# Performance work log

Measured on AMD Instinct MI355X. Metric: run time of the kernel, lower is better.

## Reference

```python
import jax, jax.numpy as jnp
import numpy as np

EMBED = 1024
HEADS = 16
HEAD_DIM = EMBED // HEADS
FFN_DIM = 4096
SEQ = 2048
BATCH = 2
EPS = 1e-5


def setup_inputs() -> dict:
    key = jax.random.key(0)
    ks = jax.random.split(key, 13)
    s = lambda n: 1.0 / np.sqrt(n)
    return {
        "x": jax.random.normal(ks[0], (BATCH, SEQ, EMBED), jnp.float32),
        # qkv projection (stored as [in, out])
        "w_qkv": jax.random.normal(ks[1], (EMBED, 3 * EMBED), jnp.float32) * s(EMBED),
        "b_qkv": jax.random.normal(ks[2], (3 * EMBED,), jnp.float32) * 0.02,
        "w_out": jax.random.normal(ks[3], (EMBED, EMBED), jnp.float32) * s(EMBED),
        "b_out": jax.random.normal(ks[4], (EMBED,), jnp.float32) * 0.02,
        # FFN
        "w_up": jax.random.normal(ks[5], (EMBED, FFN_DIM), jnp.float32) * s(EMBED),
        "b_up": jax.random.normal(ks[6], (FFN_DIM,), jnp.float32) * 0.02,
        "w_down": jax.random.normal(ks[7], (FFN_DIM, EMBED), jnp.float32) * s(FFN_DIM),
        "b_down": jax.random.normal(ks[8], (EMBED,), jnp.float32) * 0.02,
        # LayerNorms
        "g1": jnp.ones((EMBED,), jnp.float32),
        "be1": jnp.zeros((EMBED,), jnp.float32),
        "g2": jnp.ones((EMBED,), jnp.float32),
        "be2": jnp.zeros((EMBED,), jnp.float32),
    }


def _layernorm(x, g, b):
    mu = jnp.mean(x, axis=-1, keepdims=True)
    var = jnp.mean(jnp.square(x - mu), axis=-1, keepdims=True)
    return (x - mu) * jax.lax.rsqrt(var + EPS) * g + b


def reference(x, w_qkv, b_qkv, w_out, b_out, w_up, b_up, w_down, b_down, g1, be1, g2, be2):
    B, S, E = x.shape
    qkv = (x @ w_qkv + b_qkv).reshape(B, S, 3, HEADS, HEAD_DIM)
    qkv = jnp.transpose(qkv, (2, 0, 3, 1, 4))
    q, k, v = qkv[0], qkv[1], qkv[2]
    scale = 1.0 / jnp.sqrt(jnp.float32(HEAD_DIM))
    attn = jnp.einsum("bhqd,bhkd->bhqk", q, k) * scale  # [B,H,S,S]
    causal = jnp.tril(jnp.ones((S, S), bool))
    attn = jnp.where(causal, attn, -jnp.inf)
    attn = jax.nn.softmax(attn, axis=-1)
    out = jnp.einsum("bhqk,bhkd->bhqd", attn, v)  # [B,H,S,D]
    out = jnp.transpose(out, (0, 2, 1, 3)).reshape(B, S, E)
    attn_out = out @ w_out + b_out
    x = _layernorm(x + attn_out, g1, be1)
    ffn_out = jax.nn.relu(x @ w_up + b_up) @ w_down + b_down
    return _layernorm(x + ffn_out, g2, be2)
```

## Files before the change

kernel.cpp:

```cpp
#include <hip/hip_runtime.h>
#include <hip/hip_bf16.h>

#define EMBED 1024
#define HEADS 16
#define HDIM 64
#define FFN 4096
#define SEQ 2048
#define BATCH 2
#define MTOT (BATCH*SEQ)
#define QSCALE 0.1803368801111137f

typedef __attribute__((ext_vector_type(8))) short bf16x8;
typedef __attribute__((ext_vector_type(4))) float f32x4;
typedef __attribute__((ext_vector_type(16))) float f32x16;
typedef unsigned short u16;
typedef unsigned int u32;

__device__ __forceinline__ u16 f2bf(float f) {
  union { float f; unsigned u; } v; v.f = f;
  unsigned r = v.u + 0x7FFFu + ((v.u >> 16) & 1u);
  return (u16)(r >> 16);
}

__device__ __forceinline__ void async_ld16(const void* g, void* l) {
  __builtin_amdgcn_global_load_lds((const __attribute__((address_space(1))) void*)g,
                                   (__attribute__((address_space(3))) void*)l,
                                   16, 0, 0);
}

__device__ __forceinline__ void qkv_scatter(u16* qp, u16* kp, u16* vp,
                                            int row, int col, float v) {
  const int which = col >> 10, hh = (col >> 6) & 15, d = col & 63;
  const int bb = row >> 11, ss = row & 2047;
  const int bh = bb * 16 + hh;
  if (which == 0) {
    v *= QSCALE;
    size_t idx = ((((size_t)bh * 64 + (ss >> 5)) * 4 + (d >> 4)) << 9)
               + (((ss & 31) + 32 * ((d >> 3) & 1)) << 3) + (d & 7);
    qp[idx] = f2bf(v);
  } else if (which == 1) {
    size_t idx = ((((size_t)bh * 32 + (ss >> 6)) * 8 + (d >> 4) * 2 + ((ss >> 5) & 1)) << 9)
               + (((ss & 31) + 32 * ((d >> 3) & 1)) << 3) + (d & 7);
    kp[idx] = f2bf(v);
  } else {
    size_t idx = ((((size_t)bh * 32 + (ss >> 6)) * 8 + ((ss & 63) >> 4) * 2 + (d >> 5)) << 9)
               + (((d & 31) + 32 * ((ss >> 3) & 1)) << 3) + (ss & 7);
    vp[idx] = f2bf(v);
  }
}

__global__ __launch_bounds__(256) void k_cvt(const float* __restrict__ in,
                                             u16* __restrict__ out, int n4) {
  int i = blockIdx.x * 256 + threadIdx.x;
  int st = gridDim.x * 256;
  for (; i < n4; i += st) {
    float4 v = ((const float4*)in)[i];
    ushort4 o;
    o.x = f2bf(v.x); o.y = f2bf(v.y); o.z = f2bf(v.z); o.w = f2bf(v.w);
    ((ushort4*)out)[i] = o;
  }
}

__global__ __launch_bounds__(256) void k_tr(const float* __restrict__ w,
                                            u16* __restrict__ wT, int K, int N) {
  __shared__ u16 tile[32][33];
  int n0 = blockIdx.x * 32, k0 = blockIdx.y * 32;
  int tx = threadIdx.x, ty = threadIdx.y;
  #pragma unroll
  for (int i = 0; i < 4; ++i) {
    int k = k0 + ty + i * 8;
    tile[ty + i * 8][tx] = f2bf(w[(size_t)k * N + n0 + tx]);
  }
  __syncthreads();
  #pragma unroll
  for (int i = 0; i < 4; ++i) {
    int n = n0 + ty + i * 8;
    wT[(size_t)n * K + k0 + tx] = tile[tx][ty + i * 8];
  }
}

template <int OMODE, bool RELU>
__global__ __launch_bounds__(512) void k_gemm8(
    const u16* __restrict__ A, const u16* __restrict__ BT,
    const float* __restrict__ bias,
    void* __restrict__ out0, void* __restrict__ out1, void* __restrict__ out2,
    int M, int N, int K, int ldk) {
  __shared__ __align__(16) u16 As[2][2][128 * 64];
  __shared__ __align__(16) u16 Bs[2][2][128 * 64];
  const int tid = threadIdx.x;
  const int lane = tid & 63, g = lane >> 4, li = lane & 15;
  const int wid = tid >> 6, wm = wid >> 2, wn = wid & 3;

  const int gx = gridDim.x;
  const int nwg = gx * gridDim.y;
  const int flat = blockIdx.y * gx + blockIdx.x;
  const int cpx = nwg >> 3;
  const int swz = (flat & 7) * cpx + (flat >> 3);
  const int m0 = (swz / gx) * 256, n0 = (swz % gx) * 256;
  const int kchunk = blockIdx.z * K;

  f32x4 acc[8][4] = {};

  const u16* Ablk = A + (size_t)m0 * ldk + kchunk;
  const u16* Bblk = BT + (size_t)n0 * ldk + kchunk;
  const int trow = tid >> 3;
  const int sc = (tid & 7) ^ (trow & 7);

  auto stageA = [&](int buf, int h, int kt) {
    #pragma unroll
    for (int r = 0; r < 2; ++r)
      async_ld16(Ablk + (size_t)(h * 64 + r * 128 + trow) * ldk + kt + sc * 8,
                 &As[buf][h][0] + r * 4096 + tid * 8);
  };
  auto stageB = [&](int buf, int h, int kt) {
    #pragma unroll
    for (int r = 0; r < 2; ++r) {
      const int p = trow + r * 64;
      async_ld16(Bblk + (size_t)(((p >> 5) << 6) + h * 32 + (p & 31)) * ldk + kt + sc * 8,
                 &Bs[buf][h][0] + r * 4096 + tid * 8);
    }
  };

#define VM4_ asm volatile("s_waitcnt vmcnt(4)" ::: "memory")
#define VM2_ asm volatile("s_waitcnt vmcnt(2)" ::: "memory")
#define VM0_ asm volatile("s_waitcnt vmcnt(0)" ::: "memory")
#define VMN_
#define GP8(IH, JH, VMSTMT, STAGE_STMT) do {                                   \
    bf16x8 a_[4][2], b_[2][2];                                                 \
    _Pragma("unroll")                                                          \
    for (int i2 = 0; i2 < 4; ++i2) {                                           \
      const int pa = wm * 64 + i2 * 16 + li;                                   \
      _Pragma("unroll")                                                        \
      for (int ks = 0; ks < 2; ++ks)                                           \
        a_[i2][ks] = *(const bf16x8*)(&As[cur][IH][0] + pa * 64 +              \
                                      (((ks * 4 + g) ^ (li & 7)) * 8));        \
    }                                                                          \
    _Pragma("unroll")                                                          \
    for (int j2 = 0; j2 < 2; ++j2) {                                           \
      const int pb = wn * 32 + j2 * 16 + li;                                   \
      _Pragma("unroll")                                                        \
      for (int ks = 0; ks < 2; ++ks)                                           \
        b_[j2][ks] = *(const bf16x8*)(&Bs[cur][JH][0] + pb * 64 +              \
                                      (((ks * 4 + g) ^ (li & 7)) * 8));        \
    }                                                                          \
    STAGE_STMT;                                                                \
    VMSTMT;                                                                    \
    __builtin_amdgcn_s_barrier();                                              \
    asm volatile("s_waitcnt lgkmcnt(0)" ::: "memory");                         \
    __builtin_amdgcn_sched_barrier(0);                                         \
    __builtin_amdgcn_s_setprio(1);                                             \
    _Pragma("unroll")                                                          \
    for (int ks = 0; ks < 2; ++ks)                                             \
      _Pragma("unroll")                                                        \
      for (int i2 = 0; i2 < 4; ++i2)                                           \
        _Pragma("unroll")                                                      \
        for (int j2 = 0; j2 < 2; ++j2)                                         \
          acc[IH * 4 + i2][JH * 2 + j2] = __builtin_amdgcn_mfma_f32_16x16x32_bf16( \
              a_[i2][ks], b_[j2][ks], acc[IH * 4 + i2][JH * 2 + j2], 0, 0, 0); \
    __builtin_amdgcn_s_setprio(0);                                             \
    asm volatile("" ::: "memory");                                             \
  } while (0)

  stageA(0, 0, 0); stageB(0, 0, 0); stageA(0, 1, 0); stageB(0, 1, 0);
  VM4_;
  __builtin_amdgcn_s_barrier();
  asm volatile("" ::: "memory");

  int cur = 0;
  const int nkt = K >> 6;
  for (int t = 0; t < nkt - 1; ++t) {
    const int kn = (t + 1) * 64;
    GP8(0, 0, VM4_, stageA(cur ^ 1, 0, kn));
    GP8(1, 0, VM4_, stageB(cur ^ 1, 0, kn));
    GP8(0, 1, VMN_, stageA(cur ^ 1, 1, kn));
    GP8(1, 1, VM4_, stageB(cur ^ 1, 1, kn));
    cur ^= 1;
  }
  GP8(0, 0, VM2_, );
  GP8(1, 0, VM0_, );
  GP8(0, 1, VMN_, );
  GP8(1, 1, VMN_, );
#undef GP8
#undef VM4_
#undef VM2_
#undef VM0_
#undef VMN_

  float bcol[4];
  #pragma unroll
  for (int j = 0; j < 4; ++j)
    bcol[j] = (OMODE == 3) ? 0.f : bias[n0 + wn * 64 + j * 16 + li];

  #pragma unroll
  for (int i = 0; i < 8; ++i) {
    #pragma unroll
    for (int j = 0; j < 4; ++j) {
      #pragma unroll
      for (int r = 0; r < 4; ++r) {
        int row = m0 + wm * 128 + i * 16 + g * 4 + r;
        int col = n0 + wn * 64 + j * 16 + li;
        float v = acc[i][j][r] + bcol[j];
        if (RELU) v = fmaxf(v, 0.f);
        if (OMODE == 0) {
          ((u16*)out0)[(size_t)row * N + col] = f2bf(v);
        } else if (OMODE == 3) {
          ((float*)out0)[(size_t)blockIdx.z * M * N + (size_t)row * N + col] = v;
        } else {
          qkv_scatter((u16*)out0, (u16*)out1, (u16*)out2, row, col, v);
        }
      }
    }
  }
}

template <bool RELU>
__global__ __launch_bounds__(512) void k_gemmD(
    const u16* __restrict__ A, const u16* __restrict__ BT,
    const float* __restrict__ bias, float* __restrict__ out,
    int M, int N, int K) {
  __shared__ __align__(16) u16 As[4][2][64 * 64];
  __shared__ __align__(16) u16 Bs[4][2][64 * 64];
  const int tid = threadIdx.x;
  const int lane = tid & 63, g = lane >> 4, li = lane & 15;
  const int wid = tid >> 6, wm = wid >> 2, wn = wid & 3;

  const int gx = gridDim.x;
  const int nwg = gx * gridDim.y;
  const int flat = blockIdx.y * gx + blockIdx.x;
  const int cpx = nwg >> 3;
  const int swz = (flat & 7) * cpx + (flat >> 3);
  const int m0 = (swz / gx) * 128, n0 = (swz % gx) * 128;

  f32x4 acc[4][2] = {};

  const u16* Ablk = A + (size_t)m0 * K;
  const u16* Bblk = BT + (size_t)n0 * K;
  const int p = tid >> 3;
  const int c = (tid & 7) ^ (p & 7);

  auto stageAll = [&](int buf, int kt) {
    {
      const int grow = (p >> 5) * 64 + 0 * 32 + (p & 31);
      async_ld16(Ablk + (size_t)grow * K + kt + c * 8, &As[buf][0][0] + tid * 8);
    }
    {
      const int grow = (p >> 4) * 32 + 0 * 16 + (p & 15);
      async_ld16(Bblk + (size_t)grow * K + kt + c * 8, &Bs[buf][0][0] + tid * 8);
    }
    {
      const int grow = (p >> 4) * 32 + 1 * 16 + (p & 15);
      async_ld16(Bblk + (size_t)grow * K + kt + c * 8, &Bs[buf][1][0] + tid * 8);
    }
    {
      const int grow = (p >> 5) * 64 + 1 * 32 + (p & 31);
      async_ld16(Ablk + (size_t)grow * K + kt + c * 8, &As[buf][1][0] + tid * 8);
    }
  };

#define GATE(n) asm volatile("s_waitcnt vmcnt(" #n ")" ::: "memory")
  stageAll(0, 0);
  stageAll(1, 64);
  GATE(5);
  __builtin_amdgcn_s_barrier();
  asm volatile("" ::: "memory");

  const int nkt = K >> 6;
  const int pa0 = wm * 32 + li, pa1 = wm * 32 + 16 + li;
  const int pb = wn * 16 + li;
  for (int t = 0; t < nkt; ++t) {
    const int buf = t & 3;
    bf16x8 a_[2][2], b_[2][2];
    #pragma unroll
    for (int ks = 0; ks < 2; ++ks) {
      a_[0][ks] = *(const bf16x8*)(&As[buf][0][0] + pa0 * 64 + (((ks * 4 + g) ^ (pa0 & 7)) * 8));
      a_[1][ks] = *(const bf16x8*)(&As[buf][0][0] + pa1 * 64 + (((ks * 4 + g) ^ (pa1 & 7)) * 8));
      b_[0][ks] = *(const bf16x8*)(&Bs[buf][0][0] + pb * 64 + (((ks * 4 + g) ^ (pb & 7)) * 8));
      b_[1][ks] = *(const bf16x8*)(&Bs[buf][1][0] + pb * 64 + (((ks * 4 + g) ^ (pb & 7)) * 8));
    }
    if (t + 2 < nkt) {
      stageAll((t + 2) & 3, (t + 2) * 64);
      GATE(8);
    } else if (t + 1 < nkt) {
      GATE(4);
    } else {
      GATE(0);
    }
    __builtin_amdgcn_s_barrier();
    asm volatile("s_waitcnt lgkmcnt(0)" ::: "memory");
    __builtin_amdgcn_sched_barrier(0);
    __builtin_amdgcn_s_setprio(1);
    #pragma unroll
    for (int ks = 0; ks < 2; ++ks)
      #pragma unroll
      for (int i2l = 0; i2l < 2; ++i2l)
        #pragma unroll
        for (int j2 = 0; j2 < 2; ++j2)
          acc[i2l][j2] = __builtin_amdgcn_mfma_f32_16x16x32_bf16(
              a_[i2l][ks], b_[j2][ks], acc[i2l][j2], 0, 0, 0);
    __builtin_amdgcn_s_setprio(0);
    asm volatile("" ::: "memory");
    #pragma unroll
    for (int ks = 0; ks < 2; ++ks) {
      a_[0][ks] = *(const bf16x8*)(&As[buf][1][0] + pa0 * 64 + (((ks * 4 + g) ^ (pa0 & 7)) * 8));
      a_[1][ks] = *(const bf16x8*)(&As[buf][1][0] + pa1 * 64 + (((ks * 4 + g) ^ (pa1 & 7)) * 8));
    }
    if (t + 2 < nkt)      GATE(5);
    else if (t + 1 < nkt) GATE(1);
    __builtin_amdgcn_s_barrier();
    asm volatile("s_waitcnt lgkmcnt(0)" ::: "memory");
    __builtin_amdgcn_sched_barrier(0);
    __builtin_amdgcn_s_setprio(1);
    #pragma unroll
    for (int ks = 0; ks < 2; ++ks)
      #pragma unroll
      for (int i2l = 0; i2l < 2; ++i2l)
        #pragma unroll
        for (int j2 = 0; j2 < 2; ++j2)
          acc[2 + i2l][j2] = __builtin_amdgcn_mfma_f32_16x16x32_bf16(
              a_[i2l][ks], b_[j2][ks], acc[2 + i2l][j2], 0, 0, 0);
    __builtin_amdgcn_s_setprio(0);
    asm volatile("" ::: "memory");
  }
#undef GATE

  float bcol[2];
  #pragma unroll
  for (int j = 0; j < 2; ++j) bcol[j] = bias[n0 + wn * 32 + j * 16 + li];

  #pragma unroll
  for (int i = 0; i < 4; ++i) {
    #pragma unroll
    for (int j = 0; j < 2; ++j) {
      #pragma unroll
      for (int r = 0; r < 4; ++r) {
        int row = m0 + wm * 64 + i * 16 + g * 4 + r;
        int col = n0 + wn * 32 + j * 16 + li;
        float v = acc[i][j][r] + bcol[j];
        if (RELU) v = fmaxf(v, 0.f);
        out[(size_t)row * N + col] = v;
      }
    }
  }
}

__global__ __launch_bounds__(256, 3) void k_attn7(
    const u16* __restrict__ Qp, const u16* __restrict__ Kp,
    const u16* __restrict__ Vp, u16* __restrict__ ctx) {
  const int bh = blockIdx.x;
  const int t32 = 63 - (int)blockIdx.y;
  const int b = bh >> 4, h = bh & 15;
  const int tid = threadIdx.x;
  const int wid = tid >> 6, lane = tid & 63;
  const int ql = lane & 31, hl = lane >> 5;

  __shared__ __align__(16) float mrg[3][64][34];

  const int wq0 = t32 * 32;
  const int qg = wq0 + ql;
  const int nt = ((wq0 + 31) >> 6) + 1;

  bf16x8 qf[4];
  {
    const u16* qpb = Qp + ((((size_t)bh * 64 + t32) * 4) << 9) + lane * 8;
    #pragma unroll
    for (int d4 = 0; d4 < 4; ++d4)
      qf[d4] = *(const bf16x8*)(qpb + (d4 << 9));
  }

  const u16* kbase = Kp + (((size_t)bh * 32) << 12) + lane * 8;
  const u16* vbase = Vp + (((size_t)bh * 32) << 12) + lane * 8;

  f32x16 o0 = {}, o1 = {};
  float m_run = -1e30f, l_run = 0.f;

  for (int kt = wid; kt < nt; kt += 4) {
    const bool kh1 = (kt * 64 + 32 <= wq0 + 31);
    const bool domask = (kt * 64 + (kh1 ? 63 : 31) > wq0);
    const u16* kb_ = kbase + ((size_t)kt << 12);
    const u16* vb_ = vbase + ((size_t)kt << 12);

    bf16x8 kf0[4], kf1[4];
    #pragma unroll
    for (int d4 = 0; d4 < 4; ++d4) {
      kf0[d4] = *(const bf16x8*)(kb_ + ((d4 * 2 + 0) << 9));
      if (kh1) kf1[d4] = *(const bf16x8*)(kb_ + ((d4 * 2 + 1) << 9));
    }
    bf16x8 vf0[4], vf1[4];
    #pragma unroll
    for (int t = 0; t < 4; ++t)
      if (t < 2 || kh1) {
        vf0[t] = *(const bf16x8*)(vb_ + ((t * 2 + 0) << 9));
        vf1[t] = *(const bf16x8*)(vb_ + ((t * 2 + 1) << 9));
      }

    f32x16 S0 = {}, S1 = {};
    #pragma unroll
    for (int d4 = 0; d4 < 4; ++d4)
      S0 = __builtin_amdgcn_mfma_f32_32x32x16_bf16(kf0[d4], qf[d4], S0, 0, 0, 0);
    if (kh1) {
      #pragma unroll
      for (int d4 = 0; d4 < 4; ++d4)
        S1 = __builtin_amdgcn_mfma_f32_32x32x16_bf16(kf1[d4], qf[d4], S1, 0, 0, 0);
    }

    if (domask) {
      const int qrel = qg - kt * 64 - 4 * hl;
      #pragma unroll
      for (int r = 0; r < 16; ++r) {
        const int kc = (r & 3) + 8 * (r >> 2);
        S0[r] = (kc <= qrel) ? S0[r] : -3.0e38f;
      }
      if (kh1) {
        #pragma unroll
        for (int r = 0; r < 16; ++r) {
          const int kc = 32 + (r & 3) + 8 * (r >> 2);
          S1[r] = (kc <= qrel) ? S1[r] : -3.0e38f;
        }
      }
    }

    float mt = -3.0e38f;
    #pragma unroll
    for (int r = 0; r < 16; ++r) mt = fmaxf(mt, S0[r]);
    if (kh1) {
      #pragma unroll
      for (int r = 0; r < 16; ++r) mt = fmaxf(mt, S1[r]);
    }
    mt = fmaxf(mt, __shfl_xor(mt, 32, 64));

    if (!__all(mt <= m_run + 8.0f)) {
      const float mn = fmaxf(m_run, mt);
      const float alpha = exp2f(m_run - mn);
      l_run *= alpha;
      o0 *= alpha;
      o1 *= alpha;
      m_run = mn;
    }
    float sum = 0.f;
    #pragma unroll
    for (int r = 0; r < 16; ++r) { S0[r] = exp2f(S0[r] - m_run); sum += S0[r]; }
    if (kh1) {
      #pragma unroll
      for (int r = 0; r < 16; ++r) { S1[r] = exp2f(S1[r] - m_run); sum += S1[r]; }
    }
    sum += __shfl_xor(sum, 32, 64);
    l_run += sum;

    u32 pk[2][8], sw[2][8];
    #pragma unroll
    for (int m = 0; m < 4; ++m) {
      asm("v_cvt_pk_bf16_f32 %0, %1, %2" : "=v"(pk[0][2*m])   : "v"(S0[4*m+0]), "v"(S0[4*m+1]));
      asm("v_cvt_pk_bf16_f32 %0, %1, %2" : "=v"(pk[0][2*m+1]) : "v"(S0[4*m+2]), "v"(S0[4*m+3]));
    }
    #pragma unroll
    for (int i = 0; i < 8; ++i) sw[0][i] = __shfl_xor(pk[0][i], 32, 64);
    if (kh1) {
      #pragma unroll
      for (int m = 0; m < 4; ++m) {
        asm("v_cvt_pk_bf16_f32 %0, %1, %2" : "=v"(pk[1][2*m])   : "v"(S1[4*m+0]), "v"(S1[4*m+1]));
        asm("v_cvt_pk_bf16_f32 %0, %1, %2" : "=v"(pk[1][2*m+1]) : "v"(S1[4*m+2]), "v"(S1[4*m+3]));
      }
      #pragma unroll
      for (int i = 0; i < 8; ++i) sw[1][i] = __shfl_xor(pk[1][i], 32, 64);
    }

    #pragma unroll
    for (int t = 0; t < 4; ++t) {
      if (t < 2 || kh1) {
        const int c = t >> 1, m0 = 2 * (t & 1), m1 = m0 + 1;
        union { u32 u[4]; bf16x8 v; } pf;
        pf.u[0] = hl ? sw[c][2*m1]   : pk[c][2*m0];
        pf.u[1] = hl ? sw[c][2*m1+1] : pk[c][2*m0+1];
        pf.u[2] = hl ? pk[c][2*m1]   : sw[c][2*m0];
        pf.u[3] = hl ? pk[c][2*m1+1] : sw[c][2*m0+1];
        o0 = __builtin_amdgcn_mfma_f32_32x32x16_bf16(vf0[t], pf.v, o0, 0, 0, 0);
        o1 = __builtin_amdgcn_mfma_f32_32x32x16_bf16(vf1[t], pf.v, o1, 0, 0, 0);
      }
    }
  }

  if (wid > 0) {
    float* pq = &mrg[wid - 1][lane][0];
    *(f32x16*)(pq) = o0;
    *(f32x16*)(pq + 16) = o1;
    pq[32] = m_run;
    pq[33] = l_run;
  }
  __syncthreads();
  if (wid > 0) return;

  float M = m_run;
  #pragma unroll
  for (int w = 0; w < 3; ++w) M = fmaxf(M, mrg[w][lane][32]);
  const float fa = exp2f(m_run - M);
  f32x16 acc0 = o0 * fa, acc1 = o1 * fa;
  float L = l_run * fa;
  #pragma unroll
  for (int w = 0; w < 3; ++w) {
    const float* pq = &mrg[w][lane][0];
    const float fw = exp2f(pq[32] - M);
    L += pq[33] * fw;
    f32x16 t0 = *(const f32x16*)(pq);
    f32x16 t1 = *(const f32x16*)(pq + 16);
    acc0 += t0 * fw;
    acc1 += t1 * fw;
  }
  const float inv = 1.f / L;

  u16* outp = ctx + (size_t)(b * SEQ + qg) * EMBED + h * HDIM + 4 * hl;
  #pragma unroll
  for (int m = 0; m < 4; ++m) {
    ushort4 s0v, s1v;
    s0v.x = f2bf(acc0[4*m+0] * inv); s0v.y = f2bf(acc0[4*m+1] * inv);
    s0v.z = f2bf(acc0[4*m+2] * inv); s0v.w = f2bf(acc0[4*m+3] * inv);
    *(ushort4*)(outp + 8 * m) = s0v;
    s1v.x = f2bf(acc1[4*m+0] * inv); s1v.y = f2bf(acc1[4*m+1] * inv);
    s1v.z = f2bf(acc1[4*m+2] * inv); s1v.w = f2bf(acc1[4*m+3] * inv);
    *(ushort4*)(outp + 32 + 8 * m) = s1v;
  }
}

__global__ __launch_bounds__(256) void k_add_ln(
    const float* __restrict__ a, const float* __restrict__ bmat,
    const float* __restrict__ gam, const float* __restrict__ bet,
    float* __restrict__ outf, u16* __restrict__ outb) {
  const int row = blockIdx.x;
  const int t = threadIdx.x;
  __shared__ float red[8];
  float4 va = ((const float4*)(a + (size_t)row * EMBED))[t];
  float4 vb = ((const float4*)(bmat + (size_t)row * EMBED))[t];
  float s0 = va.x + vb.x, s1 = va.y + vb.y, s2 = va.z + vb.z, s3 = va.w + vb.w;
  float sum = s0 + s1 + s2 + s3;
  float sq = s0 * s0 + s1 * s1 + s2 * s2 + s3 * s3;
  #pragma unroll
  for (int m = 1; m < 64; m <<= 1) {
    sum += __shfl_xor(sum, m, 64);
    sq += __shfl_xor(sq, m, 64);
  }
  int wid = t >> 6;
  if ((t & 63) == 0) { red[wid] = sum; red[4 + wid] = sq; }
  __syncthreads();
  sum = red[0] + red[1] + red[2] + red[3];
  sq = red[4] + red[5] + red[6] + red[7];
  float mean = sum * (1.f / EMBED);
  float var = sq * (1.f / EMBED) - mean * mean;
  float rstd = rsqrtf(var + 1e-5f);
  float4 gv = ((const float4*)gam)[t], bev = ((const float4*)bet)[t];
  float y0 = (s0 - mean) * rstd * gv.x + bev.x;
  float y1 = (s1 - mean) * rstd * gv.y + bev.y;
  float y2 = (s2 - mean) * rstd * gv.z + bev.z;
  float y3 = (s3 - mean) * rstd * gv.w + bev.w;
  if (outf) {
    float4 o; o.x = y0; o.y = y1; o.z = y2; o.w = y3;
    ((float4*)(outf + (size_t)row * EMBED))[t] = o;
  }
  if (outb) {
    ushort4 ob; ob.x = f2bf(y0); ob.y = f2bf(y1); ob.z = f2bf(y2); ob.w = f2bf(y3);
    ((ushort4*)(outb + (size_t)row * EMBED))[t] = ob;
  }
}

__global__ __launch_bounds__(256) void k_add_ln4(
    const float* __restrict__ a, const float* __restrict__ parts,
    const float* __restrict__ bias,
    const float* __restrict__ gam, const float* __restrict__ bet,
    float* __restrict__ outf) {
  const int row = blockIdx.x;
  const int t = threadIdx.x;
  __shared__ float red[8];
  float4 va = ((const float4*)(a + (size_t)row * EMBED))[t];
  float4 bv = ((const float4*)bias)[t];
  float s0 = va.x + bv.x, s1 = va.y + bv.y, s2 = va.z + bv.z, s3 = va.w + bv.w;
  #pragma unroll
  for (int c = 0; c < 4; ++c) {
    float4 pv = ((const float4*)(parts + (size_t)c * MTOT * EMBED + (size_t)row * EMBED))[t];
    s0 += pv.x; s1 += pv.y; s2 += pv.z; s3 += pv.w;
  }
  float sum = s0 + s1 + s2 + s3;
  float sq = s0 * s0 + s1 * s1 + s2 * s2 + s3 * s3;
  #pragma unroll
  for (int m = 1; m < 64; m <<= 1) {
    sum += __shfl_xor(sum, m, 64);
    sq += __shfl_xor(sq, m, 64);
  }
  int wid = t >> 6;
  if ((t & 63) == 0) { red[wid] = sum; red[4 + wid] = sq; }
  __syncthreads();
  sum = red[0] + red[1] + red[2] + red[3];
  sq = red[4] + red[5] + red[6] + red[7];
  float mean = sum * (1.f / EMBED);
  float var = sq * (1.f / EMBED) - mean * mean;
  float rstd = rsqrtf(var + 1e-5f);
  float4 gv = ((const float4*)gam)[t], bev = ((const float4*)bet)[t];
  float4 o;
  o.x = (s0 - mean) * rstd * gv.x + bev.x;
  o.y = (s1 - mean) * rstd * gv.y + bev.y;
  o.z = (s2 - mean) * rstd * gv.z + bev.z;
  o.w = (s3 - mean) * rstd * gv.w + bev.w;
  ((float4*)(outf + (size_t)row * EMBED))[t] = o;
}

extern "C" void kernel_launch(void* const* d_in, const int* in_sizes, int n_in,
                              void* d_out, int out_size, void* d_ws, size_t ws_size,
                              hipStream_t stream) {
  const float* x      = (const float*)d_in[0];
  const float* w_qkv  = (const float*)d_in[1];
  const float* b_qkv  = (const float*)d_in[2];
  const float* w_out  = (const float*)d_in[3];
  const float* b_out  = (const float*)d_in[4];
  const float* w_up   = (const float*)d_in[5];
  const float* b_up   = (const float*)d_in[6];
  const float* w_down = (const float*)d_in[7];
  const float* b_down = (const float*)d_in[8];
  const float* g1  = (const float*)d_in[9];
  const float* be1 = (const float*)d_in[10];
  const float* g2  = (const float*)d_in[11];
  const float* be2 = (const float*)d_in[12];

  char* ws = (char*)d_ws;
  size_t off = 0;
  auto alloc = [&](size_t bytes) { void* p = ws + off; off += (bytes + 255) & ~(size_t)255; return p; };

  u16* xb     = (u16*)alloc((size_t)MTOT * EMBED * 2);
  u16* wqkvT  = (u16*)alloc((size_t)3 * EMBED * EMBED * 2);
  u16* woutT  = (u16*)alloc((size_t)EMBED * EMBED * 2);
  u16* wupT   = (u16*)alloc((size_t)FFN * EMBED * 2);
  u16* wdownT = (u16*)alloc((size_t)EMBED * FFN * 2);
  u16* qp     = (u16*)alloc((size_t)MTOT * EMBED * 2);
  u16* kp     = (u16*)alloc((size_t)MTOT * EMBED * 2);
  u16* vp     = (u16*)alloc((size_t)MTOT * EMBED * 2);
  u16* ctx    = (u16*)alloc((size_t)MTOT * EMBED * 2);
  float* attn_proj = (float*)alloc((size_t)MTOT * EMBED * 4);
  float* y_f32     = (float*)alloc((size_t)MTOT * EMBED * 4);
  u16* y_bf16      = (u16*)alloc((size_t)MTOT * EMBED * 2);
  u16* hmid        = (u16*)alloc((size_t)MTOT * FFN * 2);
  float* fparts    = (float*)alloc((size_t)4 * MTOT * EMBED * 4);

  dim3 trb(32, 8);
  k_cvt<<<2048, 256, 0, stream>>>(x, xb, MTOT * EMBED / 4);
  k_tr<<<dim3(3 * EMBED / 32, EMBED / 32), trb, 0, stream>>>(w_qkv, wqkvT, EMBED, 3 * EMBED);
  k_tr<<<dim3(EMBED / 32, EMBED / 32), trb, 0, stream>>>(w_out, woutT, EMBED, EMBED);
  k_tr<<<dim3(FFN / 32, EMBED / 32), trb, 0, stream>>>(w_up, wupT, EMBED, FFN);
  k_tr<<<dim3(EMBED / 32, FFN / 32), trb, 0, stream>>>(w_down, wdownT, FFN, EMBED);

  k_gemm8<2, false><<<dim3(3 * EMBED / 256, MTOT / 256), 512, 0, stream>>>(
      xb, wqkvT, b_qkv, qp, kp, vp, MTOT, 3 * EMBED, EMBED, EMBED);

  k_attn7<<<dim3(BATCH * HEADS, 64), 256, 0, stream>>>(qp, kp, vp, ctx);

  k_gemmD<false><<<dim3(EMBED / 128, MTOT / 128), 512, 0, stream>>>(
      ctx, woutT, b_out, attn_proj, MTOT, EMBED, EMBED);

  k_add_ln<<<MTOT, 256, 0, stream>>>(x, attn_proj, g1, be1, y_f32, y_bf16);

  k_gemm8<0, true><<<dim3(FFN / 256, MTOT / 256), 512, 0, stream>>>(
      y_bf16, wupT, b_up, hmid, nullptr, nullptr, MTOT, FFN, EMBED, EMBED);

  k_gemm8<3, false><<<dim3(EMBED / 256, MTOT / 256, 4), 512, 0, stream>>>(
      hmid, wdownT, nullptr, fparts, nullptr, nullptr, MTOT, EMBED, FFN / 4, FFN);

  k_add_ln4<<<MTOT, 256, 0, stream>>>(y_f32, fparts, b_down, g2, be2, (float*)d_out);

  (void)in_sizes; (void)n_in; (void)out_size; (void)ws_size;
}
```

Before: 234.8 us.

## Replace 256x256 GEMM tile with 128x128 four-wave kernel and deeper K pipeline

Swaps the 512-thread 256x256-tile GEMM for a 256-thread 128x128-tile kernel that splits each 64-wide K step into two 32-wide halves. Staging runs three half-steps ahead through a rolling double buffer with adjusted vmcnt waits. The smaller tile quadruples block count and cuts LDS use, aiming for better occupancy and CU fill on the QKV, FFN-up and split-K FFN-down GEMMs. The cost is less operand reuse per block, so each output needs more global and LDS traffic.

New measurement: 273.5 us. 16.5% more time.

```diff
diff --git a/kernel.cpp b/kernel.cpp
--- a/kernel.cpp
+++ b/kernel.cpp
@@ -80,68 +80,61 @@
 }
 
 template <int OMODE, bool RELU>
-__global__ __launch_bounds__(512) void k_gemm8(
+__global__ __launch_bounds__(256) void k_gemmL(
     const u16* __restrict__ A, const u16* __restrict__ BT,
     const float* __restrict__ bias,
     void* __restrict__ out0, void* __restrict__ out1, void* __restrict__ out2,
     int M, int N, int K, int ldk) {
-  __shared__ __align__(16) u16 As[2][2][128 * 64];
-  __shared__ __align__(16) u16 Bs[2][2][128 * 64];
+  __shared__ __align__(16) u16 As[2][2][128 * 32];
+  __shared__ __align__(16) u16 Bs[2][2][128 * 32];
   const int tid = threadIdx.x;
   const int lane = tid & 63, g = lane >> 4, li = lane & 15;
-  const int wid = tid >> 6, wm = wid >> 2, wn = wid & 3;
+  const int wid = tid >> 6, wm = wid >> 1, wn = wid & 1;
 
   const int gx = gridDim.x;
   const int nwg = gx * gridDim.y;
   const int flat = blockIdx.y * gx + blockIdx.x;
   const int cpx = nwg >> 3;
   const int swz = (flat & 7) * cpx + (flat >> 3);
-  const int m0 = (swz / gx) * 256, n0 = (swz % gx) * 256;
+  const int m0 = (swz / gx) * 128, n0 = (swz % gx) * 128;
   const int kchunk = blockIdx.z * K;
 
-  f32x4 acc[8][4] = {};
+  f32x4 acc[4][4] = {};
 
   const u16* Ablk = A + (size_t)m0 * ldk + kchunk;
   const u16* Bblk = BT + (size_t)n0 * ldk + kchunk;
-  const int trow = tid >> 3;
-  const int sc = (tid & 7) ^ (trow & 7);
-
-  auto stageA = [&](int buf, int h, int kt) {
-    #pragma unroll
-    for (int r = 0; r < 2; ++r)
-      async_ld16(Ablk + (size_t)(h * 64 + r * 128 + trow) * ldk + kt + sc * 8,
-                 &As[buf][h][0] + r * 4096 + tid * 8);
+  const int trow = tid >> 2;
+  const int tc = tid & 3;
+
+  auto stage = [&](int buf, int kh, int kt) {
+    #pragma unroll
+    for (int r = 0; r < 2; ++r) {
+      const int row = r * 64 + trow;
+      const int sc = tc ^ (row & 3);
+      async_ld16(Ablk + (size_t)row * ldk + kt + kh * 32 + sc * 8,
+                 &As[buf][kh][0] + r * 2048 + tid * 8);
+      async_ld16(Bblk + (size_t)row * ldk + kt + kh * 32 + sc * 8,
+                 &Bs[buf][kh][0] + r * 2048 + tid * 8);
+    }
   };
-  auto stageB = [&](int buf, int h, int kt) {
-    #pragma unroll
-    for (int r = 0; r < 2; ++r) {
-      const int p = trow + r * 64;
-      async_ld16(Bblk + (size_t)(((p >> 5) << 6) + h * 32 + (p & 31)) * ldk + kt + sc * 8,
-                 &Bs[buf][h][0] + r * 4096 + tid * 8);
-    }
-  };
-
+
+#define VM8_ asm volatile("s_waitcnt vmcnt(8)" ::: "memory")
 #define VM4_ asm volatile("s_waitcnt vmcnt(4)" ::: "memory")
-#define VM2_ asm volatile("s_waitcnt vmcnt(2)" ::: "memory")
 #define VM0_ asm volatile("s_waitcnt vmcnt(0)" ::: "memory")
 #define VMN_
-#define GP8(IH, JH, VMSTMT, STAGE_STMT) do {                                   \
-    bf16x8 a_[4][2], b_[2][2];                                                 \
+#define PHL(KH, VMSTMT, STAGE_STMT) do {                                       \
+    bf16x8 a_[4], b_[4];                                                       \
     _Pragma("unroll")                                                          \
     for (int i2 = 0; i2 < 4; ++i2) {                                           \
       const int pa = wm * 64 + i2 * 16 + li;                                   \
-      _Pragma("unroll")                                                        \
-      for (int ks = 0; ks < 2; ++ks)                                           \
-        a_[i2][ks] = *(const bf16x8*)(&As[cur][IH][0] + pa * 64 +              \
-                                      (((ks * 4 + g) ^ (li & 7)) * 8));        \
+      a_[i2] = *(const bf16x8*)(&As[cur][KH][0] + pa * 32 +                    \
+                                ((g ^ (pa & 3)) * 8));                         \
     }                                                                          \
     _Pragma("unroll")                                                          \
-    for (int j2 = 0; j2 < 2; ++j2) {                                           \
-      const int pb = wn * 32 + j2 * 16 + li;                                   \
-      _Pragma("unroll")                                                        \
-      for (int ks = 0; ks < 2; ++ks)                                           \
-        b_[j2][ks] = *(const bf16x8*)(&Bs[cur][JH][0] + pb * 64 +              \
-                                      (((ks * 4 + g) ^ (li & 7)) * 8));        \
+    for (int j2 = 0; j2 < 4; ++j2) {                                           \
+      const int pb = wn * 64 + j2 * 16 + li;                                   \
+      b_[j2] = *(const bf16x8*)(&Bs[cur][KH][0] + pb * 32 +                    \
+                                ((g ^ (pb & 3)) * 8));                         \
     }                                                                          \
     STAGE_STMT;                                                                \
     VMSTMT;                                                                    \
@@ -150,39 +143,33 @@
     __builtin_amdgcn_sched_barrier(0);                                         \
     __builtin_amdgcn_s_setprio(1);                                             \
     _Pragma("unroll")                                                          \
-    for (int ks = 0; ks < 2; ++ks)                                             \
+    for (int i2 = 0; i2 < 4; ++i2)                                             \
       _Pragma("unroll")                                                        \
-      for (int i2 = 0; i2 < 4; ++i2)                                           \
-        _Pragma("unroll")                                                      \
-        for (int j2 = 0; j2 < 2; ++j2)                                         \
-          acc[IH * 4 + i2][JH * 2 + j2] = __builtin_amdgcn_mfma_f32_16x16x32_bf16( \
-              a_[i2][ks], b_[j2][ks], acc[IH * 4 + i2][JH * 2 + j2], 0, 0, 0); \
+      for (int j2 = 0; j2 < 4; ++j2)                                           \
+        acc[i2][j2] = __builtin_amdgcn_mfma_f32_16x16x32_bf16(                 \
+            a_[i2], b_[j2], acc[i2][j2], 0, 0, 0);                             \
     __builtin_amdgcn_s_setprio(0);                                             \
     asm volatile("" ::: "memory");                                             \
   } while (0)
 
-  stageA(0, 0, 0); stageB(0, 0, 0); stageA(0, 1, 0); stageB(0, 1, 0);
-  VM4_;
+  stage(0, 0, 0); stage(0, 1, 0); stage(1, 0, 64);
+  VM8_;
   __builtin_amdgcn_s_barrier();
   asm volatile("" ::: "memory");
 
   int cur = 0;
   const int nkt = K >> 6;
-  for (int t = 0; t < nkt - 1; ++t) {
-    const int kn = (t + 1) * 64;
-    GP8(0, 0, VM4_, stageA(cur ^ 1, 0, kn));
-    GP8(1, 0, VM4_, stageB(cur ^ 1, 0, kn));
-    GP8(0, 1, VMN_, stageA(cur ^ 1, 1, kn));
-    GP8(1, 1, VM4_, stageB(cur ^ 1, 1, kn));
+  for (int t = 0; t < nkt; ++t) {
+    if (t + 1 < nkt) { PHL(0, VM8_, stage(cur ^ 1, 1, (t + 1) * 64)); }
+    else             { PHL(0, VM0_, ); }
+    if (t + 2 < nkt)      { PHL(1, VM8_, stage(cur, 0, (t + 2) * 64)); }
+    else if (t + 1 < nkt) { PHL(1, VM4_, ); }
+    else                  { PHL(1, VMN_, ); }
     cur ^= 1;
   }
-  GP8(0, 0, VM2_, );
-  GP8(1, 0, VM0_, );
-  GP8(0, 1, VMN_, );
-  GP8(1, 1, VMN_, );
-#undef GP8
+#undef PHL
+#undef VM8_
 #undef VM4_
-#undef VM2_
 #undef VM0_
 #undef VMN_
 
@@ -192,12 +179,12 @@
     bcol[j] = (OMODE == 3) ? 0.f : bias[n0 + wn * 64 + j * 16 + li];
 
   #pragma unroll
-  for (int i = 0; i < 8; ++i) {
+  for (int i = 0; i < 4; ++i) {
     #pragma unroll
     for (int j = 0; j < 4; ++j) {
       #pragma unroll
       for (int r = 0; r < 4; ++r) {
-        int row = m0 + wm * 128 + i * 16 + g * 4 + r;
+        int row = m0 + wm * 64 + i * 16 + g * 4 + r;
         int col = n0 + wn * 64 + j * 16 + li;
         float v = acc[i][j][r] + bcol[j];
         if (RELU) v = fmaxf(v, 0.f);
@@ -643,7 +630,7 @@
   k_tr<<<dim3(FFN / 32, EMBED / 32), trb, 0, stream>>>(w_up, wupT, EMBED, FFN);
   k_tr<<<dim3(EMBED / 32, FFN / 32), trb, 0, stream>>>(w_down, wdownT, FFN, EMBED);
 
-  k_gemm8<2, false><<<dim3(3 * EMBED / 256, MTOT / 256), 512, 0, stream>>>(
+  k_gemmL<2, false><<<dim3(3 * EMBED / 128, MTOT / 128), 256, 0, stream>>>(
       xb, wqkvT, b_qkv, qp, kp, vp, MTOT, 3 * EMBED, EMBED, EMBED);
 
   k_attn7<<<dim3(BATCH * HEADS, 64), 256, 0, stream>>>(qp, kp, vp, ctx);
@@ -653,10 +640,10 @@
 
   k_add_ln<<<MTOT, 256, 0, stream>>>(x, attn_proj, g1, be1, y_f32, y_bf16);
 
-  k_gemm8<0, true><<<dim3(FFN / 256, MTOT / 256), 512, 0, stream>>>(
+  k_gemmL<0, true><<<dim3(FFN / 128, MTOT / 128), 256, 0, stream>>>(
       y_bf16, wupT, b_up, hmid, nullptr, nullptr, MTOT, FFN, EMBED, EMBED);
 
-  k_gemm8<3, false><<<dim3(EMBED / 256, MTOT / 256, 4), 512, 0, stream>>>(
+  k_gemmL<3, false><<<dim3(EMBED / 128, MTOT / 128, 4), 256, 0, stream>>>(
       hmid, wdownT, nullptr, fparts, nullptr, nullptr, MTOT, EMBED, FFN / 4, FFN);
 
   k_add_ln4<<<MTOT, 256, 0, stream>>>(y_f32, fparts, b_down, g2, be2, (float*)d_out);
```
